# Performance work log

Measured on AMD Instinct MI355X. Metric: run time of the kernel, lower is better.

Reference implementation:

```python
import jax, jax.numpy as jnp
import numpy as np

WS = 8            # window size (square)
NUM_HEADS = 8
DIM = 256
IMG = 256         # feature map H=W for mask construction
SHIFT = WS // 2
B = 4


def _rel_pos_index(Wh, Ww):
    coords = np.stack(np.meshgrid(np.arange(Wh), np.arange(Ww), indexing='ij'))  # (2,Wh,Ww)
    cf = coords.reshape(2, -1)
    rel = cf[:, :, None] - cf[:, None, :]        # (2,N,N)
    rel = rel.transpose(1, 2, 0).astype(np.int64)
    rel[..., 0] += Wh - 1
    rel[..., 1] += Ww - 1
    rel[..., 0] *= 2 * Ww - 1
    return rel.sum(-1)                           # (N,N)


def _shift_mask(H, W, ws, ss):
    # standard Swin shifted-window attention mask: (nW, ws*ws, ws*ws) with 0 / -100
    img = np.zeros((H, W), dtype=np.float32)
    cnt = 0
    for hs in (slice(0, -ws), slice(-ws, -ss), slice(-ss, None)):
        for wsl in (slice(0, -ws), slice(-ws, -ss), slice(-ss, None)):
            img[hs, wsl] = cnt
            cnt += 1
    m = img.reshape(H // ws, ws, W // ws, ws).transpose(0, 2, 1, 3).reshape(-1, ws * ws)
    am = m[:, None, :] - m[:, :, None]
    return np.where(am != 0, np.float32(-100.0), np.float32(0.0))


def setup_inputs() -> dict:
    key = jax.random.key(0)
    ks = jax.random.split(key, 10)
    nW = (IMG // WS) ** 2
    B_ = B * nW
    N = WS * WS
    x = jax.random.normal(ks[0], (B_, N, DIM), dtype=jnp.float32)
    y = jax.random.normal(ks[1], (B_, N, DIM), dtype=jnp.float32)
    mask = jnp.asarray(_shift_mask(IMG, IMG, WS, SHIFT))
    s = 0.02
    q_w = jax.random.normal(ks[2], (DIM, DIM), dtype=jnp.float32) * s
    q_b = jnp.zeros((DIM,), dtype=jnp.float32)
    kv_w = jax.random.normal(ks[3], (2 * DIM, DIM), dtype=jnp.float32) * s
    kv_b = jnp.zeros((2 * DIM,), dtype=jnp.float32)
    proj_w = jax.random.normal(ks[4], (DIM, DIM), dtype=jnp.float32) * s
    proj_b = jnp.zeros((DIM,), dtype=jnp.float32)
    rpb_table = jax.random.normal(ks[5], ((2 * WS - 1) ** 2, NUM_HEADS), dtype=jnp.float32) * s
    return {"x": x, "y": y, "mask": mask, "q_w": q_w, "q_b": q_b,
            "kv_w": kv_w, "kv_b": kv_b, "proj_w": proj_w, "proj_b": proj_b,
            "rpb_table": rpb_table}


def reference(x, y, mask, q_w, q_b, kv_w, kv_b, proj_w, proj_b, rpb_table):
    B_, N, C = x.shape
    H = NUM_HEADS
    hd = C // H
    scale = hd ** -0.5
    # projections
    q = (x @ q_w.T + q_b).reshape(B_, N, H, hd).transpose(0, 2, 1, 3) * scale  # (B_,H,N,hd)
    kv = (y @ kv_w.T + kv_b).reshape(B_, N, 2, H, hd)
    k = kv[:, :, 0].transpose(0, 2, 1, 3)  # (B_,H,N,hd)
    v = kv[:, :, 1].transpose(0, 2, 1, 3)
    attn = jnp.einsum('bhid,bhjd->bhij', q, k)  # (B_,H,N,N)
    # relative position bias gathered from table
    rpi = jnp.asarray(_rel_pos_index(WS, WS))           # (N,N) int
    bias = rpb_table[rpi.reshape(-1)].reshape(N, N, H).transpose(2, 0, 1)  # (H,N,N)
    attn = attn + bias[None]
    # shifted-window mask
    nW = mask.shape[0]
    attn = attn.reshape(B_ // nW, nW, H, N, N) + mask[None, :, None]
    attn = attn.reshape(B_, H, N, N)
    attn = jax.nn.softmax(attn, axis=-1)
    out = jnp.einsum('bhij,bhjd->bhid', attn, v)        # (B_,H,N,hd)
    out = out.transpose(0, 2, 1, 3).reshape(B_, N, C)
    return out @ proj_w.T + proj_b
```

## Files before the change

kernel.cpp:

```cpp
#include <hip/hip_runtime.h>

typedef _Float16 half_t;
typedef _Float16 half8  __attribute__((ext_vector_type(8)));
typedef _Float16 half4v __attribute__((ext_vector_type(4)));
typedef float    f32x4  __attribute__((ext_vector_type(4)));

#define ROWB   528
#define VROWB  144
#define S_X    0
#define S_Y    33792
#define S_Q    67584
#define S_VT   101376
#define SMEM_BYTES 138240
#define SCALE  0.17677669529663687f

__global__ __launch_bounds__(256) void swin_prep(
    const float* __restrict__ q_w, const float* __restrict__ kv_w,
    const float* __restrict__ proj_w, const float* __restrict__ rpb,
    half_t* __restrict__ w16, float* __restrict__ bias_exp)
{
    int t = blockIdx.x * 256 + threadIdx.x;
    if (t < 65536)        w16[t] = (half_t)q_w[t];
    else if (t < 196608)  w16[t] = (half_t)kv_w[t - 65536];
    else if (t < 262144)  w16[t] = (half_t)proj_w[t - 196608];
    else {
        int u = t - 262144;
        int h = u >> 12, rest = u & 4095, i = rest >> 6, j = rest & 63;
        int idx = ((i >> 3) - (j >> 3) + 7) * 15 + ((i & 7) - (j & 7) + 7);
        bias_exp[u] = rpb[idx * 8 + h];
    }
}

__global__ __launch_bounds__(512) void swin_main(
    const float* __restrict__ x, const float* __restrict__ y,
    const float* __restrict__ mask,
    const float* __restrict__ q_b, const float* __restrict__ kv_b,
    const float* __restrict__ proj_b,
    const half_t* __restrict__ w16, const float* __restrict__ bias_exp,
    float* __restrict__ out)
{
    __shared__ __align__(16) char sm[SMEM_BYTES];
    const int tid  = threadIdx.x;
    const int w    = tid >> 6;
    const int lane = tid & 63;
    const int l15  = lane & 15;
    const int g    = lane >> 4;
    const int b    = blockIdx.x;

    const float* xb = x + (size_t)b * 16384;
    const float* yb = y + (size_t)b * 16384;

    #pragma unroll
    for (int it = 0; it < 4; ++it) {
        int c = tid + it * 512;
        int row = c >> 5, c8 = c & 31;
        float4 a0 = *(const float4*)(xb + row * 256 + c8 * 8);
        float4 a1 = *(const float4*)(xb + row * 256 + c8 * 8 + 4);
        float4 b0 = *(const float4*)(yb + row * 256 + c8 * 8);
        float4 b1 = *(const float4*)(yb + row * 256 + c8 * 8 + 4);
        half8 hx, hy;
        hx[0]=(half_t)a0.x; hx[1]=(half_t)a0.y; hx[2]=(half_t)a0.z; hx[3]=(half_t)a0.w;
        hx[4]=(half_t)a1.x; hx[5]=(half_t)a1.y; hx[6]=(half_t)a1.z; hx[7]=(half_t)a1.w;
        hy[0]=(half_t)b0.x; hy[1]=(half_t)b0.y; hy[2]=(half_t)b0.z; hy[3]=(half_t)b0.w;
        hy[4]=(half_t)b1.x; hy[5]=(half_t)b1.y; hy[6]=(half_t)b1.z; hy[7]=(half_t)b1.w;
        int off = row * ROWB + c8 * 16;
        *(half8*)(sm + S_X + off) = hx;
        *(half8*)(sm + S_Y + off) = hy;
    }
    __syncthreads();

    {
        const half_t* wq = w16;
        const int jf0 = w * 32;
        f32x4 acc[4][2];
        #pragma unroll
        for (int mt = 0; mt < 4; ++mt)
            #pragma unroll
            for (int nt = 0; nt < 2; ++nt) { f32x4 z = {0.f,0.f,0.f,0.f}; acc[mt][nt] = z; }
        #pragma unroll
        for (int kc = 0; kc < 8; ++kc) {
            int k0 = kc * 32 + g * 8;
            half8 a[4];
            #pragma unroll
            for (int mt = 0; mt < 4; ++mt)
                a[mt] = *(const half8*)(sm + S_X + (mt * 16 + l15) * ROWB + k0 * 2);
            half8 bf[2];
            #pragma unroll
            for (int nt = 0; nt < 2; ++nt)
                bf[nt] = *(const half8*)(wq + (jf0 + nt * 16 + l15) * 256 + k0);
            #pragma unroll
            for (int mt = 0; mt < 4; ++mt)
                #pragma unroll
                for (int nt = 0; nt < 2; ++nt)
                    acc[mt][nt] = __builtin_amdgcn_mfma_f32_16x16x32_f16(a[mt], bf[nt], acc[mt][nt], 0, 0, 0);
        }
        #pragma unroll
        for (int nt = 0; nt < 2; ++nt) {
            int jf = jf0 + nt * 16 + l15;
            float qb_ = q_b[jf];
            #pragma unroll
            for (int mt = 0; mt < 4; ++mt)
                #pragma unroll
                for (int r = 0; r < 4; ++r) {
                    int i = mt * 16 + g * 4 + r;
                    *(half_t*)(sm + S_Q + i * ROWB + jf * 2) = (half_t)((acc[mt][nt][r] + qb_) * SCALE);
                }
        }
    }
    __syncthreads();

    {
        const half_t* wkv = w16 + 65536;
        const int jf0 = w * 32;
        f32x4 ak[4][2], av[4][2];
        #pragma unroll
        for (int mt = 0; mt < 4; ++mt)
            #pragma unroll
            for (int nt = 0; nt < 2; ++nt) {
                f32x4 z = {0.f,0.f,0.f,0.f}; ak[mt][nt] = z; av[mt][nt] = z;
            }
        #pragma unroll
        for (int kc = 0; kc < 8; ++kc) {
            int k0 = kc * 32 + g * 8;
            half8 a[4];
            #pragma unroll
            for (int mt = 0; mt < 4; ++mt)
                a[mt] = *(const half8*)(sm + S_Y + (mt * 16 + l15) * ROWB + k0 * 2);
            half8 bk[2], bv[2];
            #pragma unroll
            for (int nt = 0; nt < 2; ++nt) {
                int jf = jf0 + nt * 16 + l15;
                bk[nt] = *(const half8*)(wkv + jf * 256 + k0);
                bv[nt] = *(const half8*)(wkv + (256 + jf) * 256 + k0);
            }
            #pragma unroll
            for (int mt = 0; mt < 4; ++mt)
                #pragma unroll
                for (int nt = 0; nt < 2; ++nt) {
                    ak[mt][nt] = __builtin_amdgcn_mfma_f32_16x16x32_f16(a[mt], bk[nt], ak[mt][nt], 0, 0, 0);
                    av[mt][nt] = __builtin_amdgcn_mfma_f32_16x16x32_f16(a[mt], bv[nt], av[mt][nt], 0, 0, 0);
                }
        }
        #pragma unroll
        for (int nt = 0; nt < 2; ++nt) {
            int jf = jf0 + nt * 16 + l15;
            float kb = kv_b[jf];
            #pragma unroll
            for (int mt = 0; mt < 4; ++mt)
                #pragma unroll
                for (int r = 0; r < 4; ++r) {
                    int i = mt * 16 + g * 4 + r;
                    *(half_t*)(sm + S_X + i * ROWB + jf * 2) = (half_t)(ak[mt][nt][r] + kb);
                }
        }
        #pragma unroll
        for (int nt = 0; nt < 2; ++nt) {
            int jf = jf0 + nt * 16 + l15;
            float vb = kv_b[256 + jf];
            #pragma unroll
            for (int mt = 0; mt < 4; ++mt) {
                int i0 = mt * 16 + g * 4;
                half4v hv;
                hv[0] = (half_t)(av[mt][nt][0] + vb);
                hv[1] = (half_t)(av[mt][nt][1] + vb);
                hv[2] = (half_t)(av[mt][nt][2] + vb);
                hv[3] = (half_t)(av[mt][nt][3] + vb);
                *(half4v*)(sm + S_VT + jf * VROWB + i0 * 2) = hv;
            }
        }
    }
    __syncthreads();

    {
        const int h = w;
        const float* mw = mask + (size_t)(b & 1023) * 4096;
        const float* be = bias_exp + h * 4096;
        const int k0 = h * 32 + g * 8;

        half8 ka[4], qf[4];
        #pragma unroll
        for (int mt = 0; mt < 4; ++mt)
            ka[mt] = *(const half8*)(sm + S_X + (mt * 16 + l15) * ROWB + k0 * 2);
        #pragma unroll
        for (int nt = 0; nt < 4; ++nt)
            qf[nt] = *(const half8*)(sm + S_Q + (nt * 16 + l15) * ROWB + k0 * 2);
        f32x4 t[4][4];
        #pragma unroll
        for (int mt = 0; mt < 4; ++mt)
            #pragma unroll
            for (int nt = 0; nt < 4; ++nt) {
                f32x4 z = {0.f,0.f,0.f,0.f};
                t[mt][nt] = __builtin_amdgcn_mfma_f32_16x16x32_f16(ka[mt], qf[nt], z, 0, 0, 0);
            }

        #pragma unroll
        for (int nt = 0; nt < 4; ++nt) {
            int i = nt * 16 + l15;
            #pragma unroll
            for (int mt = 0; mt < 4; ++mt) {
                int j0 = mt * 16 + g * 4;
                float4 mv = *(const float4*)(mw + i * 64 + j0);
                float4 bv = *(const float4*)(be + i * 64 + j0);
                t[mt][nt][0] += mv.x + bv.x;
                t[mt][nt][1] += mv.y + bv.y;
                t[mt][nt][2] += mv.z + bv.z;
                t[mt][nt][3] += mv.w + bv.w;
            }
            float m = -1e30f;
            #pragma unroll
            for (int mt = 0; mt < 4; ++mt)
                #pragma unroll
                for (int r = 0; r < 4; ++r) m = fmaxf(m, t[mt][nt][r]);
            m = fmaxf(m, __shfl_xor(m, 16));
            m = fmaxf(m, __shfl_xor(m, 32));
            float s = 0.f;
            #pragma unroll
            for (int mt = 0; mt < 4; ++mt)
                #pragma unroll
                for (int r = 0; r < 4; ++r) {
                    float p = __expf(t[mt][nt][r] - m);
                    t[mt][nt][r] = p;
                    s += p;
                }
            s += __shfl_xor(s, 16);
            s += __shfl_xor(s, 32);
            float inv = 1.f / s;
            #pragma unroll
            for (int mt = 0; mt < 4; ++mt)
                #pragma unroll
                for (int r = 0; r < 4; ++r) t[mt][nt][r] *= inv;
        }

        #pragma unroll
        for (int nt = 0; nt < 4; ++nt) {
            int i = nt * 16 + l15;
            #pragma unroll
            for (int mt = 0; mt < 4; ++mt) {
                int jc = (mt & 1) * 16 + g * 4;
                int base = (mt < 2) ? S_Q : S_X;
                half4v pv;
                pv[0] = (half_t)t[mt][nt][0];
                pv[1] = (half_t)t[mt][nt][1];
                pv[2] = (half_t)t[mt][nt][2];
                pv[3] = (half_t)t[mt][nt][3];
                *(half4v*)(sm + base + i * ROWB + (h * 32 + jc) * 2) = pv;
            }
        }
        asm volatile("s_waitcnt lgkmcnt(0)" ::: "memory");

        f32x4 o[2][4];
        #pragma unroll
        for (int dt = 0; dt < 2; ++dt)
            #pragma unroll
            for (int nt = 0; nt < 4; ++nt) { f32x4 z = {0.f,0.f,0.f,0.f}; o[dt][nt] = z; }
        #pragma unroll
        for (int kc = 0; kc < 2; ++kc) {
            int jb = g * 8;
            half8 va[2];
            #pragma unroll
            for (int dt = 0; dt < 2; ++dt) {
                int fr = h * 32 + dt * 16 + l15;
                va[dt] = *(const half8*)(sm + S_VT + fr * VROWB + (kc * 32 + jb) * 2);
            }
            int base = kc ? S_X : S_Q;
            half8 pf[4];
            #pragma unroll
            for (int nt = 0; nt < 4; ++nt)
                pf[nt] = *(const half8*)(sm + base + (nt * 16 + l15) * ROWB + (h * 32 + jb) * 2);
            #pragma unroll
            for (int dt = 0; dt < 2; ++dt)
                #pragma unroll
                for (int nt = 0; nt < 4; ++nt)
                    o[dt][nt] = __builtin_amdgcn_mfma_f32_16x16x32_f16(va[dt], pf[nt], o[dt][nt], 0, 0, 0);
        }
        #pragma unroll
        for (int nt = 0; nt < 4; ++nt) {
            int i = nt * 16 + l15;
            #pragma unroll
            for (int dt = 0; dt < 2; ++dt) {
                int d0 = dt * 16 + g * 4;
                half4v ov;
                ov[0] = (half_t)o[dt][nt][0];
                ov[1] = (half_t)o[dt][nt][1];
                ov[2] = (half_t)o[dt][nt][2];
                ov[3] = (half_t)o[dt][nt][3];
                *(half4v*)(sm + S_Q + i * ROWB + (h * 32 + d0) * 2) = ov;
            }
        }
    }
    __syncthreads();

    {
        const half_t* wp = w16 + 196608;
        const int jf0 = w * 32;
        f32x4 acc[4][2];
        #pragma unroll
        for (int mt = 0; mt < 4; ++mt)
            #pragma unroll
            for (int nt = 0; nt < 2; ++nt) { f32x4 z = {0.f,0.f,0.f,0.f}; acc[mt][nt] = z; }
        #pragma unroll
        for (int kc = 0; kc < 8; ++kc) {
            int k0 = kc * 32 + g * 8;
            half8 a[4];
            #pragma unroll
            for (int mt = 0; mt < 4; ++mt)
                a[mt] = *(const half8*)(sm + S_Q + (mt * 16 + l15) * ROWB + k0 * 2);
            half8 bf[2];
            #pragma unroll
            for (int nt = 0; nt < 2; ++nt)
                bf[nt] = *(const half8*)(wp + (jf0 + nt * 16 + l15) * 256 + k0);
            #pragma unroll
            for (int mt = 0; mt < 4; ++mt)
                #pragma unroll
                for (int nt = 0; nt < 2; ++nt)
                    acc[mt][nt] = __builtin_amdgcn_mfma_f32_16x16x32_f16(a[mt], bf[nt], acc[mt][nt], 0, 0, 0);
        }
        float* ob = out + (size_t)b * 16384;
        #pragma unroll
        for (int nt = 0; nt < 2; ++nt) {
            int jf = jf0 + nt * 16 + l15;
            float pbv = proj_b[jf];
            #pragma unroll
            for (int mt = 0; mt < 4; ++mt)
                #pragma unroll
                for (int r = 0; r < 4; ++r) {
                    int i = mt * 16 + g * 4 + r;
                    ob[i * 256 + jf] = acc[mt][nt][r] + pbv;
                }
        }
    }
}

extern "C" void kernel_launch(void* const* d_in, const int* in_sizes, int n_in,
                              void* d_out, int out_size, void* d_ws, size_t ws_size,
                              hipStream_t stream) {
    const float* x      = (const float*)d_in[0];
    const float* y      = (const float*)d_in[1];
    const float* mask   = (const float*)d_in[2];
    const float* q_w    = (const float*)d_in[3];
    const float* q_b    = (const float*)d_in[4];
    const float* kv_w   = (const float*)d_in[5];
    const float* kv_b   = (const float*)d_in[6];
    const float* proj_w = (const float*)d_in[7];
    const float* proj_b = (const float*)d_in[8];
    const float* rpb    = (const float*)d_in[9];

    half_t* w16     = (half_t*)d_ws;
    float* bias_exp = (float*)((char*)d_ws + 524288);

    swin_prep<<<1152, 256, 0, stream>>>(q_w, kv_w, proj_w, rpb, w16, bias_exp);
    swin_main<<<4096, 512, 0, stream>>>(x, y, mask, q_b, kv_b, proj_b,
                                        w16, bias_exp, (float*)d_out);
}
```

Baseline: 505.7 us.

## Halve LDS footprint by keeping V in registers and reusing buffers

```diff
diff --git a/kernel.cpp b/kernel.cpp
--- a/kernel.cpp
+++ b/kernel.cpp
@@ -6,12 +6,9 @@
 typedef float    f32x4  __attribute__((ext_vector_type(4)));
 
 #define ROWB   528
-#define VROWB  144
-#define S_X    0
-#define S_Y    33792
-#define S_Q    67584
-#define S_VT   101376
-#define SMEM_BYTES 138240
+#define S_A    0
+#define S_B    33792
+#define SMEM_BYTES 67584
 #define SCALE  0.17677669529663687f
 
 __global__ __launch_bounds__(256) void swin_prep(
@@ -31,7 +28,12 @@
     }
 }
 
-__global__ __launch_bounds__(512) void swin_main(
+static __device__ __forceinline__ unsigned pk2(float a, float b) {
+    union { _Float16 h[2]; unsigned u; } t;
+    t.h[0] = (_Float16)a; t.h[1] = (_Float16)b; return t.u;
+}
+
+__global__ __launch_bounds__(512, 4) void swin_main(
     const float* __restrict__ x, const float* __restrict__ y,
     const float* __restrict__ mask,
     const float* __restrict__ q_b, const float* __restrict__ kv_b,
@@ -46,6 +48,7 @@
     const int l15  = lane & 15;
     const int g    = lane >> 4;
     const int b    = blockIdx.x;
+    const int jf0  = w * 32;
 
     const float* xb = x + (size_t)b * 16384;
     const float* yb = y + (size_t)b * 16384;
@@ -64,68 +67,28 @@
         hy[0]=(half_t)b0.x; hy[1]=(half_t)b0.y; hy[2]=(half_t)b0.z; hy[3]=(half_t)b0.w;
         hy[4]=(half_t)b1.x; hy[5]=(half_t)b1.y; hy[6]=(half_t)b1.z; hy[7]=(half_t)b1.w;
         int off = row * ROWB + c8 * 16;
-        *(half8*)(sm + S_X + off) = hx;
-        *(half8*)(sm + S_Y + off) = hy;
+        *(half8*)(sm + S_A + off) = hx;
+        *(half8*)(sm + S_B + off) = hy;
     }
     __syncthreads();
 
+    unsigned vp[4][2][2];
     {
-        const half_t* wq = w16;
-        const int jf0 = w * 32;
-        f32x4 acc[4][2];
-        #pragma unroll
-        for (int mt = 0; mt < 4; ++mt)
-            #pragma unroll
-            for (int nt = 0; nt < 2; ++nt) { f32x4 z = {0.f,0.f,0.f,0.f}; acc[mt][nt] = z; }
+        const half_t* wkv = w16 + 65536;
+        f32x4 ak[4][2], av[4][2];
+        #pragma unroll
+        for (int mt = 0; mt < 4; ++mt)
+            #pragma unroll
+            for (int nt = 0; nt < 2; ++nt) {
+                f32x4 z = {0.f,0.f,0.f,0.f}; ak[mt][nt] = z; av[mt][nt] = z;
+            }
         #pragma unroll
         for (int kc = 0; kc < 8; ++kc) {
             int k0 = kc * 32 + g * 8;
             half8 a[4];
             #pragma unroll
             for (int mt = 0; mt < 4; ++mt)
-                a[mt] = *(const half8*)(sm + S_X + (mt * 16 + l15) * ROWB + k0 * 2);
-            half8 bf[2];
-            #pragma unroll
-            for (int nt = 0; nt < 2; ++nt)
-                bf[nt] = *(const half8*)(wq + (jf0 + nt * 16 + l15) * 256 + k0);
-            #pragma unroll
-            for (int mt = 0; mt < 4; ++mt)
-                #pragma unroll
-                for (int nt = 0; nt < 2; ++nt)
-                    acc[mt][nt] = __builtin_amdgcn_mfma_f32_16x16x32_f16(a[mt], bf[nt], acc[mt][nt], 0, 0, 0);
-        }
-        #pragma unroll
-        for (int nt = 0; nt < 2; ++nt) {
-            int jf = jf0 + nt * 16 + l15;
-            float qb_ = q_b[jf];
-            #pragma unroll
-            for (int mt = 0; mt < 4; ++mt)
-                #pragma unroll
-                for (int r = 0; r < 4; ++r) {
-                    int i = mt * 16 + g * 4 + r;
-                    *(half_t*)(sm + S_Q + i * ROWB + jf * 2) = (half_t)((acc[mt][nt][r] + qb_) * SCALE);
-                }
-        }
-    }
-    __syncthreads();
-
-    {
-        const half_t* wkv = w16 + 65536;
-        const int jf0 = w * 32;
-        f32x4 ak[4][2], av[4][2];
-        #pragma unroll
-        for (int mt = 0; mt < 4; ++mt)
-            #pragma unroll
-            for (int nt = 0; nt < 2; ++nt) {
-                f32x4 z = {0.f,0.f,0.f,0.f}; ak[mt][nt] = z; av[mt][nt] = z;
-            }
-        #pragma unroll
-        for (int kc = 0; kc < 8; ++kc) {
-            int k0 = kc * 32 + g * 8;
-            half8 a[4];
-            #pragma unroll
-            for (int mt = 0; mt < 4; ++mt)
-                a[mt] = *(const half8*)(sm + S_Y + (mt * 16 + l15) * ROWB + k0 * 2);
+                a[mt] = *(const half8*)(sm + S_B + (mt * 16 + l15) * ROWB + k0 * 2);
             half8 bk[2], bv[2];
             #pragma unroll
             for (int nt = 0; nt < 2; ++nt) {
@@ -141,6 +104,8 @@
                     av[mt][nt] = __builtin_amdgcn_mfma_f32_16x16x32_f16(a[mt], bv[nt], av[mt][nt], 0, 0, 0);
                 }
         }
+        __syncthreads();
+
         #pragma unroll
         for (int nt = 0; nt < 2; ++nt) {
             int jf = jf0 + nt * 16 + l15;
@@ -150,40 +115,73 @@
                 #pragma unroll
                 for (int r = 0; r < 4; ++r) {
                     int i = mt * 16 + g * 4 + r;
-                    *(half_t*)(sm + S_X + i * ROWB + jf * 2) = (half_t)(ak[mt][nt][r] + kb);
-                }
-        }
+                    *(half_t*)(sm + S_B + i * ROWB + jf * 2) = (half_t)(ak[mt][nt][r] + kb);
+                }
+        }
+        #pragma unroll
+        for (int nt = 0; nt < 2; ++nt) {
+            float vb = kv_b[256 + jf0 + nt * 16 + l15];
+            #pragma unroll
+            for (int mt = 0; mt < 4; ++mt) {
+                vp[mt][nt][0] = pk2(av[mt][nt][0] + vb, av[mt][nt][1] + vb);
+                vp[mt][nt][1] = pk2(av[mt][nt][2] + vb, av[mt][nt][3] + vb);
+            }
+        }
+    }
+
+    {
+        const half_t* wq = w16;
+        f32x4 acc[4][2];
+        #pragma unroll
+        for (int mt = 0; mt < 4; ++mt)
+            #pragma unroll
+            for (int nt = 0; nt < 2; ++nt) { f32x4 z = {0.f,0.f,0.f,0.f}; acc[mt][nt] = z; }
+        #pragma unroll
+        for (int kc = 0; kc < 8; ++kc) {
+            int k0 = kc * 32 + g * 8;
+            half8 a[4];
+            #pragma unroll
+            for (int mt = 0; mt < 4; ++mt)
+                a[mt] = *(const half8*)(sm + S_A + (mt * 16 + l15) * ROWB + k0 * 2);
+            half8 bf[2];
+            #pragma unroll
+            for (int nt = 0; nt < 2; ++nt)
+                bf[nt] = *(const half8*)(wq + (jf0 + nt * 16 + l15) * 256 + k0);
+            #pragma unroll
+            for (int mt = 0; mt < 4; ++mt)
+                #pragma unroll
+                for (int nt = 0; nt < 2; ++nt)
+                    acc[mt][nt] = __builtin_amdgcn_mfma_f32_16x16x32_f16(a[mt], bf[nt], acc[mt][nt], 0, 0, 0);
+        }
+        __syncthreads();
+
         #pragma unroll
         for (int nt = 0; nt < 2; ++nt) {
             int jf = jf0 + nt * 16 + l15;
-            float vb = kv_b[256 + jf];
-            #pragma unroll
-            for (int mt = 0; mt < 4; ++mt) {
-                int i0 = mt * 16 + g * 4;
-                half4v hv;
-                hv[0] = (half_t)(av[mt][nt][0] + vb);
-                hv[1] = (half_t)(av[mt][nt][1] + vb);
-                hv[2] = (half_t)(av[mt][nt][2] + vb);
-                hv[3] = (half_t)(av[mt][nt][3] + vb);
-                *(half4v*)(sm + S_VT + jf * VROWB + i0 * 2) = hv;
-            }
-        }
-    }
-    __syncthreads();
+            float qb_ = q_b[jf];
+            #pragma unroll
+            for (int mt = 0; mt < 4; ++mt)
+                #pragma unroll
+                for (int r = 0; r < 4; ++r) {
+                    int i = mt * 16 + g * 4 + r;
+                    *(half_t*)(sm + S_A + i * ROWB + jf * 2) = (half_t)((acc[mt][nt][r] + qb_) * SCALE);
+                }
+        }
+    }
 
     {
         const int h = w;
         const float* mw = mask + (size_t)(b & 1023) * 4096;
         const float* be = bias_exp + h * 4096;
-        const int k0 = h * 32 + g * 8;
+        const int k0 = jf0 + g * 8;
 
         half8 ka[4], qf[4];
         #pragma unroll
         for (int mt = 0; mt < 4; ++mt)
-            ka[mt] = *(const half8*)(sm + S_X + (mt * 16 + l15) * ROWB + k0 * 2);
+            ka[mt] = *(const half8*)(sm + S_B + (mt * 16 + l15) * ROWB + k0 * 2);
         #pragma unroll
         for (int nt = 0; nt < 4; ++nt)
-            qf[nt] = *(const half8*)(sm + S_Q + (nt * 16 + l15) * ROWB + k0 * 2);
+            qf[nt] = *(const half8*)(sm + S_A + (nt * 16 + l15) * ROWB + k0 * 2);
         f32x4 t[4][4];
         #pragma unroll
         for (int mt = 0; mt < 4; ++mt)
@@ -237,14 +235,35 @@
             #pragma unroll
             for (int mt = 0; mt < 4; ++mt) {
                 int jc = (mt & 1) * 16 + g * 4;
-                int base = (mt < 2) ? S_Q : S_X;
+                int base = (mt < 2) ? S_A : S_B;
                 half4v pv;
                 pv[0] = (half_t)t[mt][nt][0];
                 pv[1] = (half_t)t[mt][nt][1];
                 pv[2] = (half_t)t[mt][nt][2];
                 pv[3] = (half_t)t[mt][nt][3];
-                *(half4v*)(sm + base + i * ROWB + (h * 32 + jc) * 2) = pv;
-            }
+                *(half4v*)(sm + base + i * ROWB + (jf0 + jc) * 2) = pv;
+            }
+        }
+
+        half8 va[2][2];
+        {
+            int srcA = ((2 * g) & 3) * 16 + l15;
+            int srcB = ((2 * g + 1) & 3) * 16 + l15;
+            int hi = g >> 1;
+            #pragma unroll
+            for (int dt = 0; dt < 2; ++dt)
+                #pragma unroll
+                for (int kc = 0; kc < 2; ++kc) {
+                    union { unsigned u[4]; half8 h; } u8;
+                    #pragma unroll
+                    for (int p = 0; p < 4; ++p) {
+                        int src = (p >> 1) ? srcB : srcA;
+                        unsigned rlo = __shfl(vp[kc * 2 + 0][dt][p & 1], src);
+                        unsigned rhi = __shfl(vp[kc * 2 + 1][dt][p & 1], src);
+                        u8.u[p] = hi ? rhi : rlo;
+                    }
+                    va[dt][kc] = u8.h;
+                }
         }
         asm volatile("s_waitcnt lgkmcnt(0)" ::: "memory");
 
@@ -256,22 +275,16 @@
         #pragma unroll
         for (int kc = 0; kc < 2; ++kc) {
             int jb = g * 8;
-            half8 va[2];
-            #pragma unroll
-            for (int dt = 0; dt < 2; ++dt) {
-                int fr = h * 32 + dt * 16 + l15;
-                va[dt] = *(const half8*)(sm + S_VT + fr * VROWB + (kc * 32 + jb) * 2);
-            }
-            int base = kc ? S_X : S_Q;
+            int base = kc ? S_B : S_A;
             half8 pf[4];
             #pragma unroll
             for (int nt = 0; nt < 4; ++nt)
-                pf[nt] = *(const half8*)(sm + base + (nt * 16 + l15) * ROWB + (h * 32 + jb) * 2);
+                pf[nt] = *(const half8*)(sm + base + (nt * 16 + l15) * ROWB + (jf0 + jb) * 2);
             #pragma unroll
             for (int dt = 0; dt < 2; ++dt)
                 #pragma unroll
                 for (int nt = 0; nt < 4; ++nt)
-                    o[dt][nt] = __builtin_amdgcn_mfma_f32_16x16x32_f16(va[dt], pf[nt], o[dt][nt], 0, 0, 0);
+                    o[dt][nt] = __builtin_amdgcn_mfma_f32_16x16x32_f16(va[dt][kc], pf[nt], o[dt][nt], 0, 0, 0);
         }
         #pragma unroll
         for (int nt = 0; nt < 4; ++nt) {
@@ -284,7 +297,7 @@
                 ov[1] = (half_t)o[dt][nt][1];
                 ov[2] = (half_t)o[dt][nt][2];
                 ov[3] = (half_t)o[dt][nt][3];
-                *(half4v*)(sm + S_Q + i * ROWB + (h * 32 + d0) * 2) = ov;
+                *(half4v*)(sm + S_A + i * ROWB + (jf0 + d0) * 2) = ov;
             }
         }
     }
@@ -292,7 +305,6 @@
 
     {
         const half_t* wp = w16 + 196608;
-        const int jf0 = w * 32;
         f32x4 acc[4][2];
         #pragma unroll
         for (int mt = 0; mt < 4; ++mt)
@@ -304,7 +316,7 @@
             half8 a[4];
             #pragma unroll
             for (int mt = 0; mt < 4; ++mt)
-                a[mt] = *(const half8*)(sm + S_Q + (mt * 16 + l15) * ROWB + k0 * 2);
+                a[mt] = *(const half8*)(sm + S_A + (mt * 16 + l15) * ROWB + k0 * 2);
             half8 bf[2];
             #pragma unroll
             for (int nt = 0; nt < 2; ++nt)
```

Result: no change. 515.7 us (+2.0%).
